# Kernel tuning notes

Measured on AMD Instinct MI355X. Metric: run time of the kernel, lower is better.

Reference implementation:

```python
import jax, jax.numpy as jnp
import numpy as np
from jax import lax

N, M, B = 512, 1024, 1024  # signal dim, atoms, batch (batch==m required by X = W @ Gamma)
POWER_ITER = 100
IHT_ITER = 50


def setup_inputs() -> dict:
    key = jax.random.key(0)
    k1, k2 = jax.random.split(key)
    Y = jax.random.normal(k1, (B, N), dtype=jnp.float32)
    W = jax.random.normal(k2, (N, M), dtype=jnp.float32)
    return {"Y": Y, "W": W, "K": 64}


def power_method(W):
    # 100 iterations of X <- X W^T W / ||.||; returns last pre-normalization norm
    # (approx largest eigenvalue of W^T W), matching PowerMethod in the source.
    X0 = jax.random.normal(jax.random.key(42), (1, W.shape[1]), dtype=W.dtype)

    def body(i, carry):
        X, _ = carry
        X2 = (X @ W.T) @ W          # [1, m]
        nm = jnp.linalg.norm(X2)
        return (X2 / nm, nm)

    _, nm = lax.fori_loop(0, POWER_ITER, body, (X0, jnp.asarray(1.0, W.dtype)))
    return nm


def hard_threshold_k(G, K):
    # keep entries strictly larger (in abs) than the (K+1)-th largest per row
    a = jnp.sort(jnp.abs(G), axis=1)[:, ::-1]   # descending per row
    T = a[:, K][:, None]                          # [B, 1]
    return G * (jnp.abs(G) > T).astype(G.dtype)


def reference(Y, W, K):
    # NormDict: column-normalize the dictionary
    W = W / jnp.linalg.norm(W, axis=0)
    c = power_method(W)
    eta = 1.0 / c
    Yn = jnp.linalg.norm(Y)

    # IHT sparse coding
    Gamma = hard_threshold_k(Y @ (eta * W), K)     # [B, m]
    residual = Gamma @ W.T - Y                      # [B, n]

    def step(carry, _):
        Gamma, residual = carry
        Gamma = hard_threshold_k(Gamma - eta * (residual @ W), K)
        residual = Gamma @ W.T - Y
        return (Gamma, residual), jnp.linalg.norm(residual) / Yn

    (Gamma, residual), norms = lax.scan(step, (Gamma, residual), None, length=IHT_ITER)

    X = W @ Gamma  # [n, m] @ [B, m] -> requires B == m, as in the torch source
    return X, Gamma, norms
```

## Files before the change

### kernel.cpp

```cpp
#include <hip/hip_runtime.h>


#define DEV __device__ __forceinline__

constexpr int Nd = 512;
constexpr int Md = 1024;
constexpr int Bd = 1024;
constexpr int Ksp = 64;
constexpr int IHT = 50;
constexpr int NBLK = 16;

DEV float wave_reduce_f(float v) {
#pragma unroll
  for (int off = 32; off > 0; off >>= 1) v += __shfl_down(v, off);
  return v;
}
DEV double wave_reduce_d(double v) {
#pragma unroll
  for (int off = 32; off > 0; off >>= 1) v += __shfl_down(v, off);
  return v;
}
DEV float rfl_f(float v) {
  return __uint_as_float(__builtin_amdgcn_readfirstlane(__float_as_uint(v)));
}

__global__ __launch_bounds__(512) void k_zero(double* dacc, int* pcnt) {
  int t = threadIdx.x;
  if (t < 51) dacc[t] = 0.0;
  pcnt[t] = 0;
}

__global__ __launch_bounds__(256) void k_colnorm(const float* __restrict__ W,
                                                 float* __restrict__ cnorm) {
  int col = blockIdx.x * 256 + threadIdx.x;
  double ss = 0.0;
  for (int i = 0; i < Nd; ++i) {
    float w = W[(size_t)i * Md + col];
    ss = fma((double)w, (double)w, ss);
  }
  cnorm[col] = (float)sqrt(ss);
}

__global__ __launch_bounds__(256) void k_normalize(const float* __restrict__ W,
                                                   const float* __restrict__ cnorm,
                                                   float* __restrict__ Wn) {
  int idx = blockIdx.x * 256 + threadIdx.x;
  Wn[idx] = W[idx] / cnorm[idx & (Md - 1)];
}

__global__ __launch_bounds__(256) void k_yn2(const float* __restrict__ Y,
                                             double* __restrict__ dacc) {
  double s = 0.0;
  for (int i = blockIdx.x * 256 + threadIdx.x; i < Bd * Nd; i += gridDim.x * 256) {
    float y = Y[i];
    s = fma((double)y, (double)y, s);
  }
  s = wave_reduce_d(s);
  __shared__ double red[4];
  int lane = threadIdx.x & 63, wid = threadIdx.x >> 6;
  if (lane == 0) red[wid] = s;
  __syncthreads();
  if (threadIdx.x == 0) atomicAdd(&dacc[0], red[0] + red[1] + red[2] + red[3]);
}

template <int BM, int BN, int TN>
__global__ __launch_bounds__(256) void k_gemm_t(const float* __restrict__ A, int lda, int ta,
                                                const float* __restrict__ B, int ldb, int tb,
                                                float* __restrict__ C, int ldc, int Kd,
                                                float scale) {
  constexpr int AE = 32 * BM / 256;
  constexpr int BE = 32 * BN / 256;
  __shared__ __align__(16) float As[32][BM + 4];
  __shared__ __align__(16) float Bs[32][BN + 4];
  const int tid = threadIdx.x;
  const int tx = tid % (BN / TN), ty = tid / (BN / TN);
  const int m0 = blockIdx.y * BM, n0 = blockIdx.x * BN;
  float ra[AE], rb[BE];
  float acc[4][TN];
#pragma unroll
  for (int i = 0; i < 4; ++i)
#pragma unroll
    for (int j = 0; j < TN; ++j) acc[i][j] = 0.f;

  auto loadA = [&](int k0) {
    if (!ta) {
      const int c = tid & 31, r0 = tid >> 5;
#pragma unroll
      for (int i = 0; i < AE; ++i)
        ra[i] = A[(size_t)(m0 + r0 + i * 8) * lda + (k0 + c)];
    } else {
      const int r = tid % BM, c0 = tid / BM;
#pragma unroll
      for (int i = 0; i < AE; ++i)
        ra[i] = A[(size_t)(k0 + c0 + i * (256 / BM)) * lda + (m0 + r)];
    }
  };
  auto storeA = [&]() {
    if (!ta) {
      const int c = tid & 31, r0 = tid >> 5;
#pragma unroll
      for (int i = 0; i < AE; ++i) As[c][r0 + i * 8] = ra[i];
    } else {
      const int r = tid % BM, c0 = tid / BM;
#pragma unroll
      for (int i = 0; i < AE; ++i) As[c0 + i * (256 / BM)][r] = ra[i];
    }
  };
  auto loadB = [&](int k0) {
    if (!tb) {
      const int c = tid % BN, r0 = tid / BN;
#pragma unroll
      for (int i = 0; i < BE; ++i)
        rb[i] = B[(size_t)(k0 + r0 + i * (256 / BN)) * ldb + (n0 + c)];
    } else {
      const int r = tid & 31, c0 = tid >> 5;
#pragma unroll
      for (int i = 0; i < BE; ++i)
        rb[i] = B[(size_t)(n0 + c0 + i * 8) * ldb + (k0 + r)];
    }
  };
  auto storeB = [&]() {
    if (!tb) {
      const int c = tid % BN, r0 = tid / BN;
#pragma unroll
      for (int i = 0; i < BE; ++i) Bs[r0 + i * (256 / BN)][c] = rb[i];
    } else {
      const int r = tid & 31, c0 = tid >> 5;
#pragma unroll
      for (int i = 0; i < BE; ++i) Bs[r][c0 + i * 8] = rb[i];
    }
  };

  loadA(0);
  loadB(0);
  storeA();
  storeB();
  __syncthreads();
  for (int k0 = 0; k0 < Kd; k0 += 32) {
    const bool more = (k0 + 32) < Kd;
    if (more) { loadA(k0 + 32); loadB(k0 + 32); }
#pragma unroll
    for (int kk = 0; kk < 32; ++kk) {
      const float4 a4 = *(const float4*)&As[kk][ty * 4];
      const float aa[4] = {a4.x, a4.y, a4.z, a4.w};
      float bb[TN];
      if constexpr (TN == 4) {
        const float4 b4 = *(const float4*)&Bs[kk][tx * 4];
        bb[0] = b4.x; bb[1] = b4.y; bb[2] = b4.z; bb[3] = b4.w;
      } else {
        const float2 b2 = *(const float2*)&Bs[kk][tx * 2];
        bb[0] = b2.x; bb[1] = b2.y;
      }
#pragma unroll
      for (int i = 0; i < 4; ++i)
#pragma unroll
        for (int j = 0; j < TN; ++j) acc[i][j] = fmaf(aa[i], bb[j], acc[i][j]);
    }
    if (more) {
      __syncthreads();
      storeA();
      storeB();
      __syncthreads();
    }
  }
#pragma unroll
  for (int i = 0; i < 4; ++i) {
    if constexpr (TN == 4) {
      float4 o;
      o.x = acc[i][0] * scale; o.y = acc[i][1] * scale;
      o.z = acc[i][2] * scale; o.w = acc[i][3] * scale;
      *(float4*)&C[(size_t)(m0 + ty * 4 + i) * ldc + n0 + tx * 4] = o;
    } else {
      float2 o;
      o.x = acc[i][0] * scale; o.y = acc[i][1] * scale;
      *(float2*)&C[(size_t)(m0 + ty * 4 + i) * ldc + n0 + tx * 2] = o;
    }
  }
}

DEV float erfinv_xla(float x) {
  float w = -log1pf(-x * x);
  float p;
  if (w < 5.0f) {
    w = w - 2.5f;
    p = 2.81022636e-08f;
    p = fmaf(p, w, 3.43273939e-07f);
    p = fmaf(p, w, -3.5233877e-06f);
    p = fmaf(p, w, -4.39150654e-06f);
    p = fmaf(p, w, 0.00021858087f);
    p = fmaf(p, w, -0.00125372503f);
    p = fmaf(p, w, -0.00417768164f);
    p = fmaf(p, w, 0.246640727f);
    p = fmaf(p, w, 1.50140941f);
  } else {
    w = sqrtf(w) - 3.0f;
    p = -0.000200214257f;
    p = fmaf(p, w, 0.000100950558f);
    p = fmaf(p, w, 0.00134934322f);
    p = fmaf(p, w, -0.00367342844f);
    p = fmaf(p, w, 0.00573950773f);
    p = fmaf(p, w, -0.0076224613f);
    p = fmaf(p, w, 0.00943887047f);
    p = fmaf(p, w, 1.00167406f);
    p = fmaf(p, w, 2.83297682f);
  }
  return p * x;
}

#define TF_ROUND(r)                                  \
  {                                                  \
    x0 += x1;                                        \
    x1 = (x1 << (r)) | (x1 >> (32 - (r)));           \
    x1 ^= x0;                                        \
  }

__global__ __launch_bounds__(512) void k_power(const float* __restrict__ Wn,
                                               const float* __restrict__ S2,
                                               const float* __restrict__ Smat,
                                               float* __restrict__ V,
                                               float* __restrict__ cbuf,
                                               int* __restrict__ pcnt) {
  __shared__ float xbuf[Md];
  __shared__ double r99[8], r100[8];
  const int t = threadIdx.x, lane = t & 63, wv = t >> 6;
  const int bk = blockIdx.x;

  auto flag_barrier = [&](int val) {
    __syncthreads();
    if (t == 0)
      __hip_atomic_store(&pcnt[bk * 32], val, __ATOMIC_RELEASE,
                         __HIP_MEMORY_SCOPE_AGENT);
    if (wv == 0) {
      while (true) {
        int f = (lane < NBLK)
                    ? __hip_atomic_load(&pcnt[lane * 32], __ATOMIC_ACQUIRE,
                                        __HIP_MEMORY_SCOPE_AGENT)
                    : val;
        if (__all(f >= val)) break;
        __builtin_amdgcn_s_sleep(1);
      }
    }
    __syncthreads();
  };

  {
    unsigned i = (unsigned)t;
    unsigned x0 = i, x1 = i + 512u;
    const unsigned ks0 = 0u, ks1 = 42u, ks2 = 0x1BD11BDAu ^ 42u;
    x0 += ks0; x1 += ks1;
    TF_ROUND(13) TF_ROUND(15) TF_ROUND(26) TF_ROUND(6)  x0 += ks1; x1 += ks2 + 1u;
    TF_ROUND(17) TF_ROUND(29) TF_ROUND(16) TF_ROUND(24) x0 += ks2; x1 += ks0 + 2u;
    TF_ROUND(13) TF_ROUND(15) TF_ROUND(26) TF_ROUND(6)  x0 += ks0; x1 += ks1 + 3u;
    TF_ROUND(17) TF_ROUND(29) TF_ROUND(16) TF_ROUND(24) x0 += ks1; x1 += ks2 + 4u;
    TF_ROUND(13) TF_ROUND(15) TF_ROUND(26) TF_ROUND(6)  x0 += ks2; x1 += ks0 + 5u;
    const float lo = -0.99999994f;
    const float sqrt2 = 1.41421356237f;
    {
      float f = __uint_as_float((x0 >> 9) | 0x3f800000u) - 1.0f;
      float u = fmaxf(lo, f * 2.0f + lo);
      xbuf[i] = sqrt2 * erfinv_xla(u);
    }
    {
      float f = __uint_as_float((x1 >> 9) | 0x3f800000u) - 1.0f;
      float u = fmaxf(lo, f * 2.0f + lo);
      xbuf[i + 512] = sqrt2 * erfinv_xla(u);
    }
  }
  __syncthreads();

  float* s0 = V;
  float* s1 = V + 512;
  float* v99 = V + 1024;
  float* v100 = V + 1536;
  const int w = bk * 8 + wv;
  constexpr int NW = NBLK * 8;
  constexpr int RPW = 512 / NW;

  for (int i = 0; i < RPW; ++i) {
    const int row = w + NW * i;
    const float4* wr = (const float4*)(Wn + (size_t)row * Md);
    const float4* x4 = (const float4*)xbuf;
    float s = 0.f;
#pragma unroll
    for (int e = 0; e < 4; ++e) {
      const float4 w4 = wr[lane + e * 64];
      const float4 xx = x4[lane + e * 64];
      s = fmaf(w4.x, xx.x, s); s = fmaf(w4.y, xx.y, s);
      s = fmaf(w4.z, xx.z, s); s = fmaf(w4.w, xx.w, s);
    }
    s = wave_reduce_f(s);
    if (lane == 0) s0[row] = s;
  }
  flag_barrier(1);

  const float* pin = s0;
  for (int step = 0; step < 51; ++step) {
    const float* M;
    float scale;
    float* dst;
    if (step < 49)      { M = S2;   scale = 1.0f;   dst = (step & 1) ? s0 : s1; }
    else if (step == 49){ M = Smat; scale = 0.125f; dst = v99; }
    else                { M = Smat; scale = 0.125f; dst = v100; }
    for (int i = 0; i < RPW; ++i) {
      const int row = w + NW * i;
      const float4* mr = (const float4*)(M + (size_t)row * Nd);
      const float4* v4 = (const float4*)pin;
      float s = 0.f;
#pragma unroll
      for (int e = 0; e < 2; ++e) {
        const float4 m4 = mr[lane + e * 64];
        const float4 xx = v4[lane + e * 64];
        s = fmaf(m4.x, xx.x, s); s = fmaf(m4.y, xx.y, s);
        s = fmaf(m4.z, xx.z, s); s = fmaf(m4.w, xx.w, s);
      }
      s = wave_reduce_f(s);
      if (lane == 0) dst[row] = s * scale;
    }
    flag_barrier(step + 2);
    pin = dst;
  }

  if (bk == 0) {
    double a = (double)v99[t]; a *= a;
    double b2 = (double)v100[t]; b2 *= b2;
    a = wave_reduce_d(a);
    b2 = wave_reduce_d(b2);
    if (lane == 0) { r99[wv] = a; r100[wv] = b2; }
    __syncthreads();
    if (t == 0) {
      double n99 = 0.0, n100 = 0.0;
      for (int i = 0; i < 8; ++i) { n99 += r99[i]; n100 += r100[i]; }
      float c = (float)(8.0 * sqrt(n100 / n99));
      cbuf[0] = c;
      cbuf[1] = 1.0f / c;
    }
  }
}

__global__ __launch_bounds__(256, 4) void k_iht_all(
    const float* __restrict__ Q, const float* __restrict__ YW,
    const float* __restrict__ cbuf, float* __restrict__ gdense,
    double* __restrict__ normacc) {
  __shared__ float u[Md];
  __shared__ float yws[Md];
  __shared__ float sval[Ksp];
  __shared__ int sidx[Ksp];
  __shared__ unsigned histbuf[2][4][256];
  __shared__ unsigned wred[4];
  __shared__ unsigned sel_need, sel_prefix;
  __shared__ double dred[4];
  __shared__ int scnt;

  const int t = threadIdx.x;
  const int b = blockIdx.x;
  const int lane = t & 63, wv = t >> 6;
  const float eta = cbuf[1];
  const float4 yw = ((const float4*)(YW + (size_t)b * Md))[t];
  ((float4*)yws)[t] = yw;
#pragma unroll
  for (int e = 0; e < 8; ++e) ((unsigned*)histbuf)[t + e * 256] = 0u;
  const float* Qt = Q + t * 4;

  for (int it = -1; it < IHT; ++it) {
    if (it >= 0) {
      const int cnt = scnt;
      float4 p = make_float4(0.f, 0.f, 0.f, 0.f);
      int k = 0;
      for (; k + 16 <= cnt; k += 16) {
        int ids[16];
        float gs[16];
        float4 qq[16];
#pragma unroll
        for (int j = 0; j < 16; ++j) {
          ids[j] = __builtin_amdgcn_readfirstlane(sidx[k + j]);
          gs[j] = rfl_f(sval[k + j]);
        }
#pragma unroll
        for (int j = 0; j < 16; ++j) qq[j] = *(const float4*)(Qt + (size_t)ids[j] * Md);
#pragma unroll
        for (int j = 0; j < 16; ++j) p.x = fmaf(gs[j], qq[j].x, p.x);
#pragma unroll
        for (int j = 0; j < 16; ++j) p.y = fmaf(gs[j], qq[j].y, p.y);
#pragma unroll
        for (int j = 0; j < 16; ++j) p.z = fmaf(gs[j], qq[j].z, p.z);
#pragma unroll
        for (int j = 0; j < 16; ++j) p.w = fmaf(gs[j], qq[j].w, p.w);
      }
      for (; k < cnt; ++k) {
        const int id = __builtin_amdgcn_readfirstlane(sidx[k]);
        const float g = rfl_f(sval[k]);
        const float4 q = *(const float4*)(Qt + (size_t)id * Md);
        p.x = fmaf(g, q.x, p.x); p.y = fmaf(g, q.y, p.y);
        p.z = fmaf(g, q.z, p.z); p.w = fmaf(g, q.w, p.w);
      }
      ((float4*)u)[t] = p;
      __syncthreads();
      if (it >= 1) {
        double part = 0.0;
        if (t < cnt) {
          const int id = sidx[t];
          part = (double)sval[t] * ((double)u[id] - 2.0 * (double)yws[id]);
        }
        part = wave_reduce_d(part);
        if (lane == 0) dred[wv] = part;
      }
      __syncthreads();
      if (it >= 1 && t == 0)
        atomicAdd(&normacc[it - 1], dred[0] + dred[1] + dred[2] + dred[3]);
      float4 uu;
      uu.x = -(eta * (p.x - yw.x)); uu.y = -(eta * (p.y - yw.y));
      uu.z = -(eta * (p.z - yw.z)); uu.w = -(eta * (p.w - yw.w));
      ((float4*)u)[t] = uu;
      __syncthreads();
      if (t < cnt) u[sidx[t]] += sval[t];
      __syncthreads();
    } else {
      float4 uu;
      uu.x = eta * yw.x; uu.y = eta * yw.y; uu.z = eta * yw.z; uu.w = eta * yw.w;
      ((float4*)u)[t] = uu;
      __syncthreads();
    }

    float vals[4];
    unsigned key[4];
    {
      const float4 mv = ((const float4*)u)[t];
      vals[0] = mv.x; vals[1] = mv.y; vals[2] = mv.z; vals[3] = mv.w;
#pragma unroll
      for (int e = 0; e < 4; ++e) key[e] = __float_as_uint(vals[e]) & 0x7fffffffu;
    }

    unsigned need = Ksp + 1, prefix = 0u, pmask = 0u;
#pragma unroll
    for (int pass = 3; pass >= 0; --pass) {
      const int sh = 8 * pass;
      const int pb = pass & 1;
      unsigned(*hist)[256] = histbuf[pb];
#pragma unroll
      for (int e = 0; e < 4; ++e)
        if ((key[e] & pmask) == prefix) atomicAdd(&hist[wv][(key[e] >> sh) & 255u], 1u);
      __syncthreads();
      unsigned* hz = histbuf[pb ^ 1][wv];
      hz[lane] = 0u; hz[lane + 64] = 0u; hz[lane + 128] = 0u; hz[lane + 192] = 0u;
      if (wv == 0) {
        const unsigned c0 = hist[0][lane] + hist[1][lane] + hist[2][lane] + hist[3][lane];
        const unsigned c1 = hist[0][lane + 64] + hist[1][lane + 64] + hist[2][lane + 64] + hist[3][lane + 64];
        const unsigned c2 = hist[0][lane + 128] + hist[1][lane + 128] + hist[2][lane + 128] + hist[3][lane + 128];
        const unsigned c3 = hist[0][lane + 192] + hist[1][lane + 192] + hist[2][lane + 192] + hist[3][lane + 192];
        unsigned s0 = c0, s1 = c1, s2 = c2, s3 = c3;
#pragma unroll
        for (int off = 1; off < 64; off <<= 1) {
          const unsigned y0 = __shfl_down(s0, off), y1 = __shfl_down(s1, off);
          const unsigned y2 = __shfl_down(s2, off), y3 = __shfl_down(s3, off);
          if (lane + off < 64) { s0 += y0; s1 += y1; s2 += y2; s3 += y3; }
        }
        const unsigned T1 = __builtin_amdgcn_readfirstlane(s1);
        const unsigned T2 = __builtin_amdgcn_readfirstlane(s2);
        const unsigned T3 = __builtin_amdgcn_readfirstlane(s3);
        const unsigned i0 = s0 + T1 + T2 + T3;
        const unsigned i1 = s1 + T2 + T3;
        const unsigned i2 = s2 + T3;
        const unsigned i3 = s3;
        if (i0 >= need && i0 - c0 < need) { sel_prefix = prefix | ((unsigned)lane << sh); sel_need = need - (i0 - c0); }
        if (i1 >= need && i1 - c1 < need) { sel_prefix = prefix | ((unsigned)(lane + 64) << sh); sel_need = need - (i1 - c1); }
        if (i2 >= need && i2 - c2 < need) { sel_prefix = prefix | ((unsigned)(lane + 128) << sh); sel_need = need - (i2 - c2); }
        if (i3 >= need && i3 - c3 < need) { sel_prefix = prefix | ((unsigned)(lane + 192) << sh); sel_need = need - (i3 - c3); }
      }
      __syncthreads();
      prefix = sel_prefix;
      need = sel_need;
      pmask |= (255u << sh);
    }
    const unsigned Tbits = prefix;

    unsigned keep = 0u;
    unsigned myc = 0u;
#pragma unroll
    for (int e = 0; e < 4; ++e)
      if (key[e] > Tbits) { keep |= (1u << e); ++myc; }
    unsigned x = myc;
#pragma unroll
    for (int off = 1; off < 64; off <<= 1) {
      const unsigned y = __shfl_up(x, off);
      if (lane >= off) x += y;
    }
    if (lane == 63) wred[wv] = x;
    __syncthreads();
    unsigned addlo = 0u;
    for (int w2 = 0; w2 < wv; ++w2) addlo += wred[w2];
    int base = (int)(x + addlo) - (int)myc;
#pragma unroll
    for (int e = 0; e < 4; ++e) {
      if (keep & (1u << e)) {
        sidx[base] = t * 4 + e;
        sval[base] = vals[e];
        ++base;
      }
    }
    if (t == 0) scnt = (int)(wred[0] + wred[1] + wred[2] + wred[3]);
    if (it == IHT - 1) {
      float4 g;
      g.x = (keep & 1u) ? vals[0] : 0.f;
      g.y = (keep & 2u) ? vals[1] : 0.f;
      g.z = (keep & 4u) ? vals[2] : 0.f;
      g.w = (keep & 8u) ? vals[3] : 0.f;
      ((float4*)(gdense + (size_t)b * Md))[t] = g;
    }
    __syncthreads();
  }

  const int cnt = scnt;
  if (wv == 0) {
    double part = 0.0;
    if (lane < cnt) {
      const int id = sidx[lane];
      float acc2 = 0.f;
      for (int k = 0; k < cnt; ++k)
        acc2 = fmaf(sval[k], Q[(size_t)sidx[k] * Md + id], acc2);
      part = (double)sval[lane] * ((double)acc2 - 2.0 * (double)yws[id]);
    }
    part = wave_reduce_d(part);
    if (lane == 0) atomicAdd(&normacc[IHT - 1], part);
  }
}

__global__ void k_wnorms(const double* __restrict__ dacc, float* __restrict__ onorms) {
  const int t = threadIdx.x;
  if (t < IHT) {
    const double yn2 = dacc[0];
    double r2 = yn2 + dacc[1 + t];
    if (r2 < 0.0) r2 = 0.0;
    onorms[t] = (float)(sqrt(r2) / sqrt(yn2));
  }
}

extern "C" void kernel_launch(void* const* d_in, const int* in_sizes, int n_in,
                              void* d_out, int out_size, void* d_ws, size_t ws_size,
                              hipStream_t stream) {
  (void)in_sizes; (void)n_in; (void)out_size; (void)ws_size;
  const float* Y = (const float*)d_in[0];
  const float* W = (const float*)d_in[1];
  float* out = (float*)d_out;
  float* outX = out;
  float* outG = out + Nd * Md;
  float* outN = outG + Bd * Md;

  char* wsb = (char*)d_ws;
  double* dacc = (double*)wsb;
  float* cbuf = (float*)(wsb + 512);
  float* Wn = (float*)(wsb + 1024);
  float* Q = Wn + Nd * Md;
  float* YW = Q + Md * Md;
  float* Smat = YW + Bd * Md;
  float* S2 = Smat + Nd * Nd;
  float* cnorm = S2 + Nd * Nd;
  float* V = cnorm + Md;
  int* pcnt = (int*)(V + 2048);

  k_zero<<<1, 512, 0, stream>>>(dacc, pcnt);
  k_colnorm<<<4, 256, 0, stream>>>(W, cnorm);
  k_normalize<<<2048, 256, 0, stream>>>(W, cnorm, Wn);

  k_gemm_t<64, 32, 2><<<dim3(16, 8), 256, 0, stream>>>(Wn, Md, 0, Wn, Md, 1, Smat, Nd, Md, 1.0f);
  k_gemm_t<64, 32, 2><<<dim3(16, 8), 256, 0, stream>>>(Smat, Nd, 0, Smat, Nd, 0, S2, Nd, Nd, 0.015625f);
  k_gemm_t<64, 64, 4><<<dim3(16, 16), 256, 0, stream>>>(Wn, Md, 1, Wn, Md, 0, Q, Md, Nd, 1.0f);
  k_gemm_t<64, 64, 4><<<dim3(16, 16), 256, 0, stream>>>(Y, Nd, 0, Wn, Md, 0, YW, Md, Nd, 1.0f);
  k_yn2<<<128, 256, 0, stream>>>(Y, dacc);

  k_power<<<NBLK, 512, 0, stream>>>(Wn, S2, Smat, V, cbuf, pcnt);

  k_iht_all<<<1024, 256, 0, stream>>>(Q, YW, cbuf, outG, dacc + 1);
  k_wnorms<<<1, 64, 0, stream>>>(dacc, outN);

  k_gemm_t<64, 32, 2><<<dim3(32, 8), 256, 0, stream>>>(Wn, Md, 0, outG, Md, 0, outX, Md, Md, 1.0f);
}
```

Baseline: 1.010 ms.

## Merge power iteration, Q/YW GEMMs and Y-norm into one concurrent kernel

Fuses the power-method kernel with the two independent GEMMs (Q = WnᵀWn and YW = Y·Wn) and the ||Y|| reduction into a single launch. The first 16 blocks run the power iteration while the remaining blocks do the GEMM tiles and the reduction, so the latency-bound power loop overlaps with compute-bound work. The power blocks shrink to 256 threads to match the GEMM launch shape. The flag barrier now uses relaxed loads followed by an acquire fence. The risk is that the 16 spin-waiting power blocks may not all be resident at once, or may be slowed by contention from the GEMM blocks.

```diff
diff --git a/kernel.cpp b/kernel.cpp
--- a/kernel.cpp
+++ b/kernel.cpp
@@ -48,33 +48,18 @@
   Wn[idx] = W[idx] / cnorm[idx & (Md - 1)];
 }
 
-__global__ __launch_bounds__(256) void k_yn2(const float* __restrict__ Y,
-                                             double* __restrict__ dacc) {
-  double s = 0.0;
-  for (int i = blockIdx.x * 256 + threadIdx.x; i < Bd * Nd; i += gridDim.x * 256) {
-    float y = Y[i];
-    s = fma((double)y, (double)y, s);
-  }
-  s = wave_reduce_d(s);
-  __shared__ double red[4];
-  int lane = threadIdx.x & 63, wid = threadIdx.x >> 6;
-  if (lane == 0) red[wid] = s;
-  __syncthreads();
-  if (threadIdx.x == 0) atomicAdd(&dacc[0], red[0] + red[1] + red[2] + red[3]);
-}
-
 template <int BM, int BN, int TN>
-__global__ __launch_bounds__(256) void k_gemm_t(const float* __restrict__ A, int lda, int ta,
-                                                const float* __restrict__ B, int ldb, int tb,
-                                                float* __restrict__ C, int ldc, int Kd,
-                                                float scale) {
+DEV void gemm_body(float* smem, const float* __restrict__ A, int lda, int ta,
+                   const float* __restrict__ B, int ldb, int tb,
+                   float* __restrict__ C, int ldc, int Kd, float scale,
+                   int bx, int by) {
   constexpr int AE = 32 * BM / 256;
   constexpr int BE = 32 * BN / 256;
-  __shared__ __align__(16) float As[32][BM + 4];
-  __shared__ __align__(16) float Bs[32][BN + 4];
+  float (*As)[BM + 4] = (float(*)[BM + 4])smem;
+  float (*Bs)[BN + 4] = (float(*)[BN + 4])(smem + 32 * (BM + 4));
   const int tid = threadIdx.x;
   const int tx = tid % (BN / TN), ty = tid / (BN / TN);
-  const int m0 = blockIdx.y * BM, n0 = blockIdx.x * BN;
+  const int m0 = by * BM, n0 = bx * BN;
   float ra[AE], rb[BE];
   float acc[4][TN];
 #pragma unroll
@@ -176,6 +161,16 @@
       *(float2*)&C[(size_t)(m0 + ty * 4 + i) * ldc + n0 + tx * 2] = o;
     }
   }
+}
+
+template <int BM, int BN, int TN>
+__global__ __launch_bounds__(256) void k_gemm_t(const float* __restrict__ A, int lda, int ta,
+                                                const float* __restrict__ B, int ldb, int tb,
+                                                float* __restrict__ C, int ldc, int Kd,
+                                                float scale) {
+  __shared__ __align__(16) float smem[32 * (BM + 4) + 32 * (BN + 4)];
+  gemm_body<BM, BN, TN>(smem, A, lda, ta, B, ldb, tb, C, ldc, Kd, scale,
+                        blockIdx.x, blockIdx.y);
 }
 
 DEV float erfinv_xla(float x) {
@@ -214,16 +209,49 @@
     x1 ^= x0;                                        \
   }
 
-__global__ __launch_bounds__(512) void k_power(const float* __restrict__ Wn,
-                                               const float* __restrict__ S2,
-                                               const float* __restrict__ Smat,
-                                               float* __restrict__ V,
-                                               float* __restrict__ cbuf,
-                                               int* __restrict__ pcnt) {
-  __shared__ float xbuf[Md];
-  __shared__ double r99[8], r100[8];
+__global__ __launch_bounds__(256) void k_mid(const float* __restrict__ Wn,
+                                             const float* __restrict__ Y,
+                                             const float* __restrict__ S2,
+                                             const float* __restrict__ Smat,
+                                             float* __restrict__ Q,
+                                             float* __restrict__ YW,
+                                             float* __restrict__ V,
+                                             float* __restrict__ cbuf,
+                                             int* __restrict__ pcnt,
+                                             double* __restrict__ dacc) {
+  __shared__ __align__(16) float smem[32 * 68 * 2];
+  const int blk = blockIdx.x;
   const int t = threadIdx.x, lane = t & 63, wv = t >> 6;
-  const int bk = blockIdx.x;
+
+  if (blk >= NBLK) {
+    if (blk < NBLK + 256) {
+      const int id = blk - NBLK;
+      gemm_body<64, 64, 4>(smem, Wn, Md, 1, Wn, Md, 0, Q, Md, Nd, 1.0f,
+                           id & 15, id >> 4);
+    } else if (blk < NBLK + 512) {
+      const int id = blk - NBLK - 256;
+      gemm_body<64, 64, 4>(smem, Y, Nd, 0, Wn, Md, 0, YW, Md, Nd, 1.0f,
+                           id & 15, id >> 4);
+    } else {
+      const int yb = blk - NBLK - 512;
+      double s = 0.0;
+      for (int i = yb * 256 + t; i < Bd * Nd; i += 128 * 256) {
+        float y = Y[i];
+        s = fma((double)y, (double)y, s);
+      }
+      s = wave_reduce_d(s);
+      double* red = (double*)smem;
+      if (lane == 0) red[wv] = s;
+      __syncthreads();
+      if (t == 0) atomicAdd(&dacc[0], red[0] + red[1] + red[2] + red[3]);
+    }
+    return;
+  }
+
+  float* xbuf = smem;
+  double* r99 = (double*)(smem + 1024);
+  double* r100 = r99 + 8;
+  const int bk = blk;
 
   auto flag_barrier = [&](int val) {
     __syncthreads();
@@ -233,7 +261,7 @@
     if (wv == 0) {
       while (true) {
         int f = (lane < NBLK)
-                    ? __hip_atomic_load(&pcnt[lane * 32], __ATOMIC_ACQUIRE,
+                    ? __hip_atomic_load(&pcnt[lane * 32], __ATOMIC_RELAXED,
                                         __HIP_MEMORY_SCOPE_AGENT)
                     : val;
         if (__all(f >= val)) break;
@@ -241,10 +269,12 @@
       }
     }
     __syncthreads();
+    __builtin_amdgcn_fence(__ATOMIC_ACQUIRE, "agent");
   };
 
-  {
-    unsigned i = (unsigned)t;
+#pragma unroll
+  for (int h = 0; h < 2; ++h) {
+    unsigned i = (unsigned)(t + h * 256);
     unsigned x0 = i, x1 = i + 512u;
     const unsigned ks0 = 0u, ks1 = 42u, ks2 = 0x1BD11BDAu ^ 42u;
     x0 += ks0; x1 += ks1;
@@ -272,8 +302,8 @@
   float* s1 = V + 512;
   float* v99 = V + 1024;
   float* v100 = V + 1536;
-  const int w = bk * 8 + wv;
-  constexpr int NW = NBLK * 8;
+  const int w = bk * 4 + wv;
+  constexpr int NW = NBLK * 4;
   constexpr int RPW = 512 / NW;
 
   for (int i = 0; i < RPW; ++i) {
@@ -321,11 +351,16 @@
   }
 
   if (bk == 0) {
-    double a = (double)v99[t]; a *= a;
-    double b2 = (double)v100[t]; b2 *= b2;
-    a = wave_reduce_d(a);
-    b2 = wave_reduce_d(b2);
-    if (lane == 0) { r99[wv] = a; r100[wv] = b2; }
+#pragma unroll
+    for (int h = 0; h < 2; ++h) {
+      const int cw = wv + h * 4;
+      const int idx = cw * 64 + lane;
+      double a = (double)v99[idx]; a *= a;
+      double b2 = (double)v100[idx]; b2 *= b2;
+      a = wave_reduce_d(a);
+      b2 = wave_reduce_d(b2);
+      if (lane == 0) { r99[cw] = a; r100[cw] = b2; }
+    }
     __syncthreads();
     if (t == 0) {
       double n99 = 0.0, n100 = 0.0;
@@ -563,11 +598,9 @@
 
   k_gemm_t<64, 32, 2><<<dim3(16, 8), 256, 0, stream>>>(Wn, Md, 0, Wn, Md, 1, Smat, Nd, Md, 1.0f);
   k_gemm_t<64, 32, 2><<<dim3(16, 8), 256, 0, stream>>>(Smat, Nd, 0, Smat, Nd, 0, S2, Nd, Nd, 0.015625f);
-  k_gemm_t<64, 64, 4><<<dim3(16, 16), 256, 0, stream>>>(Wn, Md, 1, Wn, Md, 0, Q, Md, Nd, 1.0f);
-  k_gemm_t<64, 64, 4><<<dim3(16, 16), 256, 0, stream>>>(Y, Nd, 0, Wn, Md, 0, YW, Md, Nd, 1.0f);
-  k_yn2<<<128, 256, 0, stream>>>(Y, dacc);
-
-  k_power<<<NBLK, 512, 0, stream>>>(Wn, S2, Smat, V, cbuf, pcnt);
+
+  k_mid<<<NBLK + 512 + 128, 256, 0, stream>>>(Wn, Y, S2, Smat, Q, YW, V, cbuf,
+                                              pcnt, dacc);
 
   k_iht_all<<<1024, 256, 0, stream>>>(Q, YW, cbuf, outG, dacc + 1);
   k_wnorms<<<1, 64, 0, stream>>>(dacc, outN);
```

Result: no change. 1.031 ms (+2.0%).
